# Performance work log

Measured on AMD Instinct MI355X. Metric: run time of the kernel, lower is better.

The kernel has to match this reference:

```python
import jax, jax.numpy as jnp
import numpy as np

N = 50176
E = 802816
G = 64
IN_DIM = 128
HID = 128
GLOB = 16
BN_EPS = 1e-5


def transformer_conv(x, src, dst, Wq, bq, Wk, bk, Wv, bv, Ws, bs):
    # PyG TransformerConv, heads=1, concat=True, root_weight=True, beta=False
    q = x @ Wq + bq          # [N, H]
    k = x @ Wk + bk          # [N, H]
    v = x @ Wv + bv          # [N, H]
    scale = 1.0 / jnp.sqrt(jnp.asarray(HID, x.dtype))
    logits = jnp.sum(q[dst] * k[src], axis=-1) * scale          # [E]
    m = jax.ops.segment_max(logits, dst, num_segments=N)        # [N]
    m = jnp.where(jnp.isfinite(m), m, 0.0)
    e = jnp.exp(logits - m[dst])                                # [E]
    s = jax.ops.segment_sum(e, dst, num_segments=N)             # [N]
    alpha = e / (s[dst] + 1e-16)                                # [E]
    agg = jax.ops.segment_sum(alpha[:, None] * v[src], dst, num_segments=N)
    return agg + x @ Ws + bs


def batch_norm(x, gamma, beta):
    mu = jnp.mean(x, axis=0)
    var = jnp.mean((x - mu) ** 2, axis=0)
    return gamma * (x - mu) / jnp.sqrt(var + BN_EPS) + beta


def setup_inputs() -> dict:
    key = jax.random.key(0)
    ks = jax.random.split(key, 32)
    d = {}
    d['x'] = jax.random.normal(ks[0], (N, IN_DIM), dtype=jnp.float32)
    d['edge_index'] = jax.random.randint(ks[1], (2, E), 0, N, dtype=jnp.int32)
    d['ptr'] = (jnp.arange(G + 1, dtype=jnp.int32) * (N // G))
    d['global_features'] = jax.random.normal(ks[2], (G, GLOB), dtype=jnp.float32)
    dims = [(IN_DIM, HID), (HID, HID)]
    ki = 3
    for l, (di, do) in enumerate(dims):
        for nm in ['Wq', 'Wk', 'Wv', 'Ws']:
            d[f'{nm}{l}'] = jax.random.normal(ks[ki], (di, do), dtype=jnp.float32) * 0.05; ki += 1
        for nm in ['bq', 'bk', 'bv', 'bs']:
            d[f'{nm}{l}'] = jnp.zeros((do,), dtype=jnp.float32)
        d[f'g{l}'] = jnp.ones((do,), dtype=jnp.float32)
        d[f'be{l}'] = jnp.zeros((do,), dtype=jnp.float32)
    d['fcW'] = jax.random.normal(ks[ki], (HID + GLOB, HID), dtype=jnp.float32) * 0.05; ki += 1
    d['fcb'] = jnp.zeros((HID,), dtype=jnp.float32)
    d['fc2W'] = jax.random.normal(ks[ki], (HID, 1), dtype=jnp.float32) * 0.05; ki += 1
    d['fc2b'] = jnp.zeros((1,), dtype=jnp.float32)
    return d


def reference(x, edge_index, ptr, global_features,
              Wq0, Wk0, Wv0, Ws0, bq0, bk0, bv0, bs0, g0, be0,
              Wq1, Wk1, Wv1, Ws1, bq1, bk1, bv1, bs1, g1, be1,
              fcW, fcb, fc2W, fc2b):
    src, dst = edge_index[0], edge_index[1]
    h = transformer_conv(x, src, dst, Wq0, bq0, Wk0, bk0, Wv0, bv0, Ws0, bs0)
    h = jax.nn.relu(batch_norm(h, g0, be0))
    h = transformer_conv(h, src, dst, Wq1, bq1, Wk1, bk1, Wv1, bv1, Ws1, bs1)
    h = jax.nn.relu(batch_norm(h, g1, be1))
    # broadcast per-graph global features to nodes using ptr boundaries
    graph_id = jnp.searchsorted(ptr, jnp.arange(N, dtype=ptr.dtype), side='right') - 1
    rep = global_features[graph_id]                              # [N, GLOB]
    h = jnp.concatenate([h, rep], axis=1)
    h = jax.nn.relu(h @ fcW + fcb)
    out = h @ fc2W + fc2b                                        # [N, 1]
    return out[:, 0]
```

## Files before the change

kernel.cpp:

```cpp
#include <hip/hip_runtime.h>
#include <math.h>

#define N_NODES 50176
#define N_EDGES 802816
#define HIDDEN  128
#define NGRAPH  64
#define BN_EPS  1e-5f
#define ATT_SCALE 0.08838834764831845f

typedef __attribute__((ext_vector_type(8))) short bf16x8;
typedef __attribute__((ext_vector_type(4))) float f32x4;

__device__ __forceinline__ float bflo(unsigned u) { return __uint_as_float(u << 16); }
__device__ __forceinline__ float bfhi(unsigned u) { return __uint_as_float(u & 0xffff0000u); }
__device__ __forceinline__ unsigned short f2bf(float f) {
    unsigned u = __float_as_uint(f);
    unsigned r = (u + 0x7fffu + ((u >> 16) & 1u)) >> 16;
    return (unsigned short)r;
}

__global__ void hist_kernel(const int* __restrict__ dst, int* __restrict__ cnt) {
    int e = blockIdx.x * 256 + threadIdx.x;
    if (e < N_EDGES) atomicAdd(&cnt[dst[e]], 1);
}

__global__ void scan1_kernel(const int* __restrict__ cnt, int* __restrict__ row_ptr,
                             int* __restrict__ bsum) {
    __shared__ int sh[256];
    int t = threadIdx.x, b = blockIdx.x;
    int base = b * 1024 + t * 4;
    int v0 = cnt[base], v1 = cnt[base + 1], v2 = cnt[base + 2], v3 = cnt[base + 3];
    int tot = v0 + v1 + v2 + v3;
    sh[t] = tot; __syncthreads();
    for (int off = 1; off < 256; off <<= 1) {
        int x = (t >= off) ? sh[t - off] : 0;
        __syncthreads();
        sh[t] += x;
        __syncthreads();
    }
    int excl = sh[t] - tot;
    row_ptr[base]     = excl;
    row_ptr[base + 1] = excl + v0;
    row_ptr[base + 2] = excl + v0 + v1;
    row_ptr[base + 3] = excl + v0 + v1 + v2;
    if (t == 255) bsum[b] = sh[255];
}

__global__ void scan2_kernel(const int* __restrict__ bsum, int* __restrict__ boff,
                             int* __restrict__ row_ptr) {
    int acc = 0;
    for (int i = 0; i < 49; i++) { boff[i] = acc; acc += bsum[i]; }
    row_ptr[N_NODES] = acc;
}

__global__ void scan3_kernel(int* __restrict__ row_ptr, int* __restrict__ cur,
                             const int* __restrict__ boff) {
    int t = threadIdx.x, b = blockIdx.x;
    int base = b * 1024 + t * 4;
    int off = boff[b];
    #pragma unroll
    for (int j = 0; j < 4; j++) {
        int v = row_ptr[base + j] + off;
        row_ptr[base + j] = v;
        cur[base + j] = v;
    }
}

__global__ void scatter_kernel(const int* __restrict__ src, const int* __restrict__ dst,
                               int* __restrict__ cur, int* __restrict__ edge_src) {
    int e = blockIdx.x * 256 + threadIdx.x;
    if (e < N_EDGES) {
        int d = dst[e];
        int slot = atomicAdd(&cur[d], 1);
        edge_src[slot] = src[e];
    }
}

__global__ void wprep_kernel(const float* __restrict__ Wq, const float* __restrict__ Wk,
                             const float* __restrict__ Wv, const float* __restrict__ Ws,
                             unsigned short* __restrict__ WT) {
    int mb = blockIdx.x;
    const float* W = (mb == 0) ? Wq : (mb == 1) ? Wk : (mb == 2) ? Wv : Ws;
    int t = threadIdx.x;
    int k = t >> 1, ch = t & 1;
    #pragma unroll 8
    for (int cc = 0; cc < 64; cc++) {
        int c = ch * 64 + cc;
        WT[((size_t)mb * 128 + c) * 128 + k] = f2bf(W[k * 128 + c]);
    }
}

__global__ __launch_bounds__(512, 4) void gemm_mfma(
    const float* __restrict__ in,
    const unsigned short* __restrict__ WT,
    const float* __restrict__ bq, const float* __restrict__ bk,
    const float* __restrict__ bv, const float* __restrict__ bs,
    float* __restrict__ qb, unsigned short* __restrict__ kvb,
    float* __restrict__ hb,
    const float* __restrict__ bnA, const float* __restrict__ bnB)
{
    __shared__ unsigned char ldsA[16384];
    __shared__ unsigned char ldsKV[32768];
    int t = threadIdx.x;
    int n0 = blockIdx.x * 64;

    {
        int r = t >> 3, seg = t & 7;
        const float* srcp = in + (size_t)(n0 + r) * 128 + seg * 16;
        float4 f0 = *reinterpret_cast<const float4*>(srcp);
        float4 f1 = *reinterpret_cast<const float4*>(srcp + 4);
        float4 f2 = *reinterpret_cast<const float4*>(srcp + 8);
        float4 f3 = *reinterpret_cast<const float4*>(srcp + 12);
        if (bnA) {
            int kb = seg * 16;
            float4 a0 = *reinterpret_cast<const float4*>(&bnA[kb]);
            float4 a1 = *reinterpret_cast<const float4*>(&bnA[kb + 4]);
            float4 a2 = *reinterpret_cast<const float4*>(&bnA[kb + 8]);
            float4 a3 = *reinterpret_cast<const float4*>(&bnA[kb + 12]);
            float4 b0 = *reinterpret_cast<const float4*>(&bnB[kb]);
            float4 b1 = *reinterpret_cast<const float4*>(&bnB[kb + 4]);
            float4 b2 = *reinterpret_cast<const float4*>(&bnB[kb + 8]);
            float4 b3 = *reinterpret_cast<const float4*>(&bnB[kb + 12]);
            f0.x = fmaxf(f0.x * a0.x + b0.x, 0.f); f0.y = fmaxf(f0.y * a0.y + b0.y, 0.f);
            f0.z = fmaxf(f0.z * a0.z + b0.z, 0.f); f0.w = fmaxf(f0.w * a0.w + b0.w, 0.f);
            f1.x = fmaxf(f1.x * a1.x + b1.x, 0.f); f1.y = fmaxf(f1.y * a1.y + b1.y, 0.f);
            f1.z = fmaxf(f1.z * a1.z + b1.z, 0.f); f1.w = fmaxf(f1.w * a1.w + b1.w, 0.f);
            f2.x = fmaxf(f2.x * a2.x + b2.x, 0.f); f2.y = fmaxf(f2.y * a2.y + b2.y, 0.f);
            f2.z = fmaxf(f2.z * a2.z + b2.z, 0.f); f2.w = fmaxf(f2.w * a2.w + b2.w, 0.f);
            f3.x = fmaxf(f3.x * a3.x + b3.x, 0.f); f3.y = fmaxf(f3.y * a3.y + b3.y, 0.f);
            f3.z = fmaxf(f3.z * a3.z + b3.z, 0.f); f3.w = fmaxf(f3.w * a3.w + b3.w, 0.f);
        }
        uint4 p0, p1;
        p0.x = (unsigned)f2bf(f0.x) | ((unsigned)f2bf(f0.y) << 16);
        p0.y = (unsigned)f2bf(f0.z) | ((unsigned)f2bf(f0.w) << 16);
        p0.z = (unsigned)f2bf(f1.x) | ((unsigned)f2bf(f1.y) << 16);
        p0.w = (unsigned)f2bf(f1.z) | ((unsigned)f2bf(f1.w) << 16);
        p1.x = (unsigned)f2bf(f2.x) | ((unsigned)f2bf(f2.y) << 16);
        p1.y = (unsigned)f2bf(f2.z) | ((unsigned)f2bf(f2.w) << 16);
        p1.z = (unsigned)f2bf(f3.x) | ((unsigned)f2bf(f3.y) << 16);
        p1.w = (unsigned)f2bf(f3.z) | ((unsigned)f2bf(f3.w) << 16);
        unsigned sw = (unsigned)((r & 7) << 4);
        *reinterpret_cast<uint4*>(&ldsA[r * 256 + (((unsigned)(seg * 32)) ^ sw)]) = p0;
        *reinterpret_cast<uint4*>(&ldsA[r * 256 + (((unsigned)(seg * 32 + 16)) ^ sw)]) = p1;
    }
    __syncthreads();

    int lane = t & 63, w = t >> 6;
    int m = w >> 1, half = w & 1;
    int lrow = lane & 15, lk = lane >> 4;

    f32x4 acc[4][4] = {};
    #pragma unroll
    for (int ks = 0; ks < 4; ks++) {
        bf16x8 bfr[4], af[4];
        #pragma unroll
        for (int j = 0; j < 4; j++) {
            int col = half * 64 + j * 16 + lrow;
            bfr[j] = *reinterpret_cast<const bf16x8*>(
                &WT[((size_t)m * 128 + col) * 128 + ks * 32 + lk * 8]);
        }
        #pragma unroll
        for (int i = 0; i < 4; i++) {
            unsigned row = (unsigned)(i * 16 + lrow);
            af[i] = *reinterpret_cast<const bf16x8*>(
                &ldsA[row * 256 + (((unsigned)(ks * 64 + lk * 16)) ^ ((row & 7) << 4))]);
        }
        #pragma unroll
        for (int i = 0; i < 4; i++)
            #pragma unroll
            for (int j = 0; j < 4; j++)
                acc[i][j] = __builtin_amdgcn_mfma_f32_16x16x32_bf16(af[i], bfr[j], acc[i][j], 0, 0, 0);
    }

    const float* bias = (m == 0) ? bq : (m == 1) ? bk : (m == 2) ? bv : bs;
    if (m == 0 || m == 3) {
        float* ob = (m == 0) ? qb : hb;
        #pragma unroll
        for (int j = 0; j < 4; j++) {
            int c = half * 64 + j * 16 + lrow;
            float bi = bias[c];
            #pragma unroll
            for (int i = 0; i < 4; i++)
                #pragma unroll
                for (int r4 = 0; r4 < 4; r4++) {
                    int row = n0 + i * 16 + lk * 4 + r4;
                    ob[(size_t)row * 128 + c] = acc[i][j][r4] + bi;
                }
        }
    } else {
        unsigned vOff = (m == 1) ? 0u : 256u;
        #pragma unroll
        for (int j = 0; j < 4; j++) {
            int c = half * 64 + j * 16 + lrow;
            float bi = bias[c];
            unsigned bir = vOff + (unsigned)c * 2;
            #pragma unroll
            for (int i = 0; i < 4; i++)
                #pragma unroll
                for (int r4 = 0; r4 < 4; r4++) {
                    unsigned row = (unsigned)(i * 16 + lk * 4 + r4);
                    unsigned sw = ((row >> 2) & 3) << 5;
                    *reinterpret_cast<unsigned short*>(&ldsKV[row * 512 + (bir ^ sw)]) =
                        f2bf(acc[i][j][r4] + bi);
                }
        }
    }
    __syncthreads();
    {
        int r = t >> 3, seg = t & 7;
        unsigned sw = (((unsigned)r >> 2) & 3) << 5;
        char* dst = (char*)(kvb + (size_t)(n0 + r) * 256) + seg * 64;
        #pragma unroll
        for (int u = 0; u < 4; u++) {
            uint4 v = *reinterpret_cast<const uint4*>(
                &ldsKV[r * 512 + (((unsigned)(seg * 64 + u * 16)) ^ sw)]);
            *reinterpret_cast<uint4*>(dst + u * 16) = v;
        }
    }
}

__global__ __launch_bounds__(256) void agg_kernel(
    const float* __restrict__ qb, const unsigned short* __restrict__ kvb,
    const int* __restrict__ row_ptr, const int* __restrict__ edge_src,
    float* __restrict__ hb)
{
    int wave = threadIdx.x >> 6, lane = threadIdx.x & 63;
    int n = blockIdx.x * 4 + wave;
    int quarter = lane >> 4, ql = lane & 15;

    float4 qa = *reinterpret_cast<const float4*>(&qb[(size_t)n * 128 + ql * 8]);
    float4 qc = *reinterpret_cast<const float4*>(&qb[(size_t)n * 128 + ql * 8 + 4]);
    int s0 = row_ptr[n], s1 = row_ptr[n + 1];

    float acc0 = 0.f, acc1 = 0.f, acc2 = 0.f, acc3 = 0.f;
    float acc4 = 0.f, acc5 = 0.f, acc6 = 0.f, acc7 = 0.f;
    float ssum = 0.f;

    for (int j0 = s0; j0 < s1; j0 += 4) {
        int j = j0 + quarter;
        bool act = (j < s1);
        int s = act ? edge_src[j] : 0;
        const uint4* kv4 = reinterpret_cast<const uint4*>(kvb + (size_t)s * 256);
        uint4 kr = kv4[ql];
        uint4 vr = kv4[16 + ql];

        float part = qa.x * bflo(kr.x) + qa.y * bfhi(kr.x)
                   + qa.z * bflo(kr.y) + qa.w * bfhi(kr.y)
                   + qc.x * bflo(kr.z) + qc.y * bfhi(kr.z)
                   + qc.z * bflo(kr.w) + qc.w * bfhi(kr.w);
        part += __shfl_xor(part, 1, 64);
        part += __shfl_xor(part, 2, 64);
        part += __shfl_xor(part, 4, 64);
        part += __shfl_xor(part, 8, 64);

        float wgt = act ? __expf(part * ATT_SCALE) : 0.f;
        ssum += wgt;
        acc0 += wgt * bflo(vr.x); acc1 += wgt * bfhi(vr.x);
        acc2 += wgt * bflo(vr.y); acc3 += wgt * bfhi(vr.y);
        acc4 += wgt * bflo(vr.z); acc5 += wgt * bfhi(vr.z);
        acc6 += wgt * bflo(vr.w); acc7 += wgt * bfhi(vr.w);
    }

    #define XRED(x) { x += __shfl_xor(x, 16, 64); x += __shfl_xor(x, 32, 64); }
    XRED(acc0) XRED(acc1) XRED(acc2) XRED(acc3)
    XRED(acc4) XRED(acc5) XRED(acc6) XRED(acc7)
    XRED(ssum)
    #undef XRED

    if (quarter == 0) {
        float inv = 1.0f / (ssum + 1e-16f);
        float4 h0 = *reinterpret_cast<float4*>(&hb[(size_t)n * 128 + ql * 8]);
        float4 h1 = *reinterpret_cast<float4*>(&hb[(size_t)n * 128 + ql * 8 + 4]);
        h0.x += acc0 * inv; h0.y += acc1 * inv; h0.z += acc2 * inv; h0.w += acc3 * inv;
        h1.x += acc4 * inv; h1.y += acc5 * inv; h1.z += acc6 * inv; h1.w += acc7 * inv;
        *reinterpret_cast<float4*>(&hb[(size_t)n * 128 + ql * 8]) = h0;
        *reinterpret_cast<float4*>(&hb[(size_t)n * 128 + ql * 8 + 4]) = h1;
    }
}

__global__ __launch_bounds__(256) void bn_stats(const float* __restrict__ h,
                                                float* __restrict__ sums,
                                                float* __restrict__ sqs) {
    int t = threadIdx.x;
    int c = t & 127;
    float s = 0.f, q = 0.f;
    int stride = gridDim.x * 256;
    for (int i = blockIdx.x * 256 + t; i < N_NODES * 128; i += stride) {
        float v = h[i];
        s += v; q += v * v;
    }
    __shared__ float sh[256], shq[256];
    sh[t] = s; shq[t] = q;
    __syncthreads();
    if (t < 128) {
        atomicAdd(&sums[c], sh[t] + sh[t + 128]);
        atomicAdd(&sqs[c],  shq[t] + shq[t + 128]);
    }
}

__global__ void bn_final(const float* __restrict__ sums, const float* __restrict__ sqs,
                         const float* __restrict__ g, const float* __restrict__ be,
                         float* __restrict__ a, float* __restrict__ b) {
    int c = threadIdx.x;
    float mean = sums[c] / (float)N_NODES;
    float var  = sqs[c] / (float)N_NODES - mean * mean;
    float inv  = rsqrtf(var + BN_EPS);
    float av   = g[c] * inv;
    a[c] = av;
    b[c] = be[c] - mean * av;
}

__global__ __launch_bounds__(256) void fc_kernel(
    const float* __restrict__ h2, const float* __restrict__ a1, const float* __restrict__ b1,
    const int* __restrict__ ptr, const float* __restrict__ gf,
    const float* __restrict__ fcW, const float* __restrict__ fcb,
    const float* __restrict__ fc2W, const float* __restrict__ fc2b,
    float* __restrict__ out)
{
    __shared__ float hc[8][144];
    __shared__ float red[8][128];
    int t = threadIdx.x;
    int nb = blockIdx.x * 8;

    {
        int node_l = t >> 5, li = t & 31;
        int n = nb + node_l;
        float4 v = *reinterpret_cast<const float4*>(&h2[(size_t)n * 128 + li * 4]);
        float4 av = *reinterpret_cast<const float4*>(&a1[li * 4]);
        float4 bv = *reinterpret_cast<const float4*>(&b1[li * 4]);
        hc[node_l][li * 4 + 0] = fmaxf(v.x * av.x + bv.x, 0.f);
        hc[node_l][li * 4 + 1] = fmaxf(v.y * av.y + bv.y, 0.f);
        hc[node_l][li * 4 + 2] = fmaxf(v.z * av.z + bv.z, 0.f);
        hc[node_l][li * 4 + 3] = fmaxf(v.w * av.w + bv.w, 0.f);
        if (li < 16) {
            int lo = 0, hi = NGRAPH;
            while (lo < hi) {
                int mid = (lo + hi + 1) >> 1;
                if (ptr[mid] <= n) lo = mid; else hi = mid - 1;
            }
            hc[node_l][128 + li] = gf[lo * 16 + li];
        }
    }
    __syncthreads();

    {
        int half = t >> 7, o = t & 127;
        float fb = fcb[o];
        float acc0 = fb, acc1 = fb, acc2 = fb, acc3 = fb;
        const float* h0 = hc[half * 4 + 0];
        const float* h1 = hc[half * 4 + 1];
        const float* h2c = hc[half * 4 + 2];
        const float* h3 = hc[half * 4 + 3];
        #pragma unroll 16
        for (int i = 0; i < 144; i++) {
            float w = fcW[i * 128 + o];
            acc0 += h0[i] * w;
            acc1 += h1[i] * w;
            acc2 += h2c[i] * w;
            acc3 += h3[i] * w;
        }
        float w2 = fc2W[o];
        red[half * 4 + 0][o] = fmaxf(acc0, 0.f) * w2;
        red[half * 4 + 1][o] = fmaxf(acc1, 0.f) * w2;
        red[half * 4 + 2][o] = fmaxf(acc2, 0.f) * w2;
        red[half * 4 + 3][o] = fmaxf(acc3, 0.f) * w2;
    }
    __syncthreads();

    {
        int node_l = t >> 5, li = t & 31;
        float s = red[node_l][li] + red[node_l][li + 32]
                + red[node_l][li + 64] + red[node_l][li + 96];
        s += __shfl_xor(s, 1, 64);
        s += __shfl_xor(s, 2, 64);
        s += __shfl_xor(s, 4, 64);
        s += __shfl_xor(s, 8, 64);
        s += __shfl_xor(s, 16, 64);
        if (li == 0) out[nb + node_l] = s + fc2b[0];
    }
}

extern "C" void kernel_launch(void* const* d_in, const int* in_sizes, int n_in,
                              void* d_out, int out_size, void* d_ws, size_t ws_size,
                              hipStream_t stream)
{
    const float* x   = (const float*)d_in[0];
    const int*   ei  = (const int*)d_in[1];
    const int*   ptr = (const int*)d_in[2];
    const float* gf  = (const float*)d_in[3];
    const float* Wq0 = (const float*)d_in[4];
    const float* Wk0 = (const float*)d_in[5];
    const float* Wv0 = (const float*)d_in[6];
    const float* Ws0 = (const float*)d_in[7];
    const float* bq0 = (const float*)d_in[8];
    const float* bk0 = (const float*)d_in[9];
    const float* bv0 = (const float*)d_in[10];
    const float* bs0 = (const float*)d_in[11];
    const float* g0  = (const float*)d_in[12];
    const float* be0 = (const float*)d_in[13];
    const float* Wq1 = (const float*)d_in[14];
    const float* Wk1 = (const float*)d_in[15];
    const float* Wv1 = (const float*)d_in[16];
    const float* Ws1 = (const float*)d_in[17];
    const float* bq1 = (const float*)d_in[18];
    const float* bk1 = (const float*)d_in[19];
    const float* bv1 = (const float*)d_in[20];
    const float* bs1 = (const float*)d_in[21];
    const float* g1  = (const float*)d_in[22];
    const float* be1 = (const float*)d_in[23];
    const float* fcW = (const float*)d_in[24];
    const float* fcb = (const float*)d_in[25];
    const float* fc2W= (const float*)d_in[26];
    const float* fc2b= (const float*)d_in[27];
    float* out = (float*)d_out;

    const int* src_p = ei;
    const int* dst_p = ei + N_EDGES;

    char* w = (char*)d_ws;
    const size_t NM = (size_t)N_NODES * 128 * sizeof(float);
    float* qb = (float*)w;                    w += NM;
    unsigned short* kvb = (unsigned short*)w; w += (size_t)N_NODES * 256 * sizeof(unsigned short);
    float* h1 = (float*)w;                    w += NM;
    float* h2 = (float*)w;                    w += NM;
    float* stats = (float*)w;                 w += 1024 * sizeof(float);
    float* sums0 = stats;
    float* sqs0  = stats + 128;
    float* sums1 = stats + 256;
    float* sqs1  = stats + 384;
    float* a0    = stats + 512;
    float* b0    = stats + 640;
    float* a1    = stats + 768;
    float* b1    = stats + 896;
    unsigned short* WT0 = (unsigned short*)w; w += (size_t)512 * 128 * sizeof(unsigned short);
    unsigned short* WT1 = (unsigned short*)w; w += (size_t)512 * 128 * sizeof(unsigned short);
    int* cnt     = (int*)w;                   w += (size_t)N_NODES * sizeof(int);
    int* row_ptr = (int*)w;                   w += (size_t)(N_NODES + 1) * sizeof(int);
    int* cur     = (int*)w;                   w += (size_t)N_NODES * sizeof(int);
    int* edge_src= (int*)w;                   w += (size_t)N_EDGES * sizeof(int);
    int* bsum    = (int*)w;                   w += 64 * sizeof(int);
    int* boff    = (int*)w;                   w += 64 * sizeof(int);

    hipMemsetAsync(cnt, 0, (size_t)N_NODES * sizeof(int), stream);
    hipMemsetAsync(stats, 0, 512 * sizeof(float), stream);

    wprep_kernel<<<4, 256, 0, stream>>>(Wq0, Wk0, Wv0, Ws0, WT0);
    wprep_kernel<<<4, 256, 0, stream>>>(Wq1, Wk1, Wv1, Ws1, WT1);

    hist_kernel<<<3136, 256, 0, stream>>>(dst_p, cnt);
    scan1_kernel<<<49, 256, 0, stream>>>(cnt, row_ptr, bsum);
    scan2_kernel<<<1, 1, 0, stream>>>(bsum, boff, row_ptr);
    scan3_kernel<<<49, 256, 0, stream>>>(row_ptr, cur, boff);
    scatter_kernel<<<3136, 256, 0, stream>>>(src_p, dst_p, cur, edge_src);

    gemm_mfma<<<784, 512, 0, stream>>>(x, WT0,
        bq0, bk0, bv0, bs0, qb, kvb, h1, nullptr, nullptr);
    agg_kernel<<<12544, 256, 0, stream>>>(qb, kvb, row_ptr, edge_src, h1);
    bn_stats<<<784, 256, 0, stream>>>(h1, sums0, sqs0);
    bn_final<<<1, 128, 0, stream>>>(sums0, sqs0, g0, be0, a0, b0);

    gemm_mfma<<<784, 512, 0, stream>>>(h1, WT1,
        bq1, bk1, bv1, bs1, qb, kvb, h2, a0, b0);
    agg_kernel<<<12544, 256, 0, stream>>>(qb, kvb, row_ptr, edge_src, h2);
    bn_stats<<<784, 256, 0, stream>>>(h2, sums1, sqs1);
    bn_final<<<1, 128, 0, stream>>>(sums1, sqs1, g1, be1, a1, b1);

    fc_kernel<<<6272, 256, 0, stream>>>(h2, a1, b1, ptr, gf,
        fcW, fcb, fc2W, fc2b, out);
}
```

Before: 519.4 us.

## Store Q as bf16, unroll edge loop, fold BN-final and scan2 into consumers

Q is now written in bf16 through an LDS staging buffer with coalesced stores, which halves Q traffic in the aggregation kernel. The aggregation loop handles two edges per quarter-wave per iteration to expose more memory-level parallelism. The bn_final and scan2 kernels are removed: the BN affine coefficients are recomputed from the raw sums in the GEMM and FC kernels, and the block-offset scan is done with wave shuffles inside scan3. bn_stats now reads float4s. Lower Q precision slightly changes numerics, and the extra syncthreads in the GEMM epilogue adds a barrier.

```diff
diff --git a/kernel.cpp b/kernel.cpp
--- a/kernel.cpp
+++ b/kernel.cpp
@@ -17,6 +17,20 @@
     unsigned u = __float_as_uint(f);
     unsigned r = (u + 0x7fffu + ((u >> 16) & 1u)) >> 16;
     return (unsigned short)r;
+}
+
+__device__ __forceinline__ void bn_ab4(const float* __restrict__ S, const float* __restrict__ Q,
+                                       const float* __restrict__ G, const float* __restrict__ BE,
+                                       int c, float4& A, float4& B) {
+    const float invN = 1.0f / (float)N_NODES;
+    float4 s = *reinterpret_cast<const float4*>(&S[c]);
+    float4 q = *reinterpret_cast<const float4*>(&Q[c]);
+    float4 g = *reinterpret_cast<const float4*>(&G[c]);
+    float4 e = *reinterpret_cast<const float4*>(&BE[c]);
+    #define BNC(x) { float mu = s.x * invN; float va = q.x * invN - mu * mu; \
+                     float iv = rsqrtf(va + BN_EPS); A.x = g.x * iv; B.x = e.x - mu * A.x; }
+    BNC(x) BNC(y) BNC(z) BNC(w)
+    #undef BNC
 }
 
 __global__ void hist_kernel(const int* __restrict__ dst, int* __restrict__ cnt) {
@@ -46,18 +60,24 @@
     if (t == 255) bsum[b] = sh[255];
 }
 
-__global__ void scan2_kernel(const int* __restrict__ bsum, int* __restrict__ boff,
-                             int* __restrict__ row_ptr) {
-    int acc = 0;
-    for (int i = 0; i < 49; i++) { boff[i] = acc; acc += bsum[i]; }
-    row_ptr[N_NODES] = acc;
-}
-
 __global__ void scan3_kernel(int* __restrict__ row_ptr, int* __restrict__ cur,
-                             const int* __restrict__ boff) {
+                             const int* __restrict__ bsum) {
+    __shared__ int sh_off;
     int t = threadIdx.x, b = blockIdx.x;
+    if (t < 64) {
+        int v = (t < 49) ? bsum[t] : 0;
+        int inc = v;
+        #pragma unroll
+        for (int o = 1; o < 64; o <<= 1) {
+            int u = __shfl_up(inc, o, 64);
+            if (t >= o) inc += u;
+        }
+        if (t == b) sh_off = inc - v;
+        if (b == 48 && t == 48) row_ptr[N_NODES] = inc;
+    }
+    __syncthreads();
+    int off = sh_off;
     int base = b * 1024 + t * 4;
-    int off = boff[b];
     #pragma unroll
     for (int j = 0; j < 4; j++) {
         int v = row_ptr[base + j] + off;
@@ -95,9 +115,10 @@
     const unsigned short* __restrict__ WT,
     const float* __restrict__ bq, const float* __restrict__ bk,
     const float* __restrict__ bv, const float* __restrict__ bs,
-    float* __restrict__ qb, unsigned short* __restrict__ kvb,
+    unsigned short* __restrict__ qbf, unsigned short* __restrict__ kvb,
     float* __restrict__ hb,
-    const float* __restrict__ bnA, const float* __restrict__ bnB)
+    const float* __restrict__ bnS, const float* __restrict__ bnQ,
+    const float* __restrict__ bnG, const float* __restrict__ bnBe)
 {
     __shared__ unsigned char ldsA[16384];
     __shared__ unsigned char ldsKV[32768];
@@ -111,16 +132,13 @@
         float4 f1 = *reinterpret_cast<const float4*>(srcp + 4);
         float4 f2 = *reinterpret_cast<const float4*>(srcp + 8);
         float4 f3 = *reinterpret_cast<const float4*>(srcp + 12);
-        if (bnA) {
+        if (bnS) {
             int kb = seg * 16;
-            float4 a0 = *reinterpret_cast<const float4*>(&bnA[kb]);
-            float4 a1 = *reinterpret_cast<const float4*>(&bnA[kb + 4]);
-            float4 a2 = *reinterpret_cast<const float4*>(&bnA[kb + 8]);
-            float4 a3 = *reinterpret_cast<const float4*>(&bnA[kb + 12]);
-            float4 b0 = *reinterpret_cast<const float4*>(&bnB[kb]);
-            float4 b1 = *reinterpret_cast<const float4*>(&bnB[kb + 4]);
-            float4 b2 = *reinterpret_cast<const float4*>(&bnB[kb + 8]);
-            float4 b3 = *reinterpret_cast<const float4*>(&bnB[kb + 12]);
+            float4 a0, b0, a1, b1, a2, b2, a3, b3;
+            bn_ab4(bnS, bnQ, bnG, bnBe, kb,      a0, b0);
+            bn_ab4(bnS, bnQ, bnG, bnBe, kb + 4,  a1, b1);
+            bn_ab4(bnS, bnQ, bnG, bnBe, kb + 8,  a2, b2);
+            bn_ab4(bnS, bnQ, bnG, bnBe, kb + 12, a3, b3);
             f0.x = fmaxf(f0.x * a0.x + b0.x, 0.f); f0.y = fmaxf(f0.y * a0.y + b0.y, 0.f);
             f0.z = fmaxf(f0.z * a0.z + b0.z, 0.f); f0.w = fmaxf(f0.w * a0.w + b0.w, 0.f);
             f1.x = fmaxf(f1.x * a1.x + b1.x, 0.f); f1.y = fmaxf(f1.y * a1.y + b1.y, 0.f);
@@ -172,9 +190,10 @@
                 acc[i][j] = __builtin_amdgcn_mfma_f32_16x16x32_bf16(af[i], bfr[j], acc[i][j], 0, 0, 0);
     }
 
+    __syncthreads();
+
     const float* bias = (m == 0) ? bq : (m == 1) ? bk : (m == 2) ? bv : bs;
-    if (m == 0 || m == 3) {
-        float* ob = (m == 0) ? qb : hb;
+    if (m == 3) {
         #pragma unroll
         for (int j = 0; j < 4; j++) {
             int c = half * 64 + j * 16 + lrow;
@@ -184,7 +203,23 @@
                 #pragma unroll
                 for (int r4 = 0; r4 < 4; r4++) {
                     int row = n0 + i * 16 + lk * 4 + r4;
-                    ob[(size_t)row * 128 + c] = acc[i][j][r4] + bi;
+                    hb[(size_t)row * 128 + c] = acc[i][j][r4] + bi;
+                }
+        }
+    } else if (m == 0) {
+        #pragma unroll
+        for (int j = 0; j < 4; j++) {
+            int c = half * 64 + j * 16 + lrow;
+            float bi = bias[c];
+            #pragma unroll
+            for (int i = 0; i < 4; i++)
+                #pragma unroll
+                for (int r4 = 0; r4 < 4; r4++) {
+                    unsigned row = (unsigned)(i * 16 + lk * 4 + r4);
+                    unsigned sw = ((row >> 2) & 3) << 5;
+                    *reinterpret_cast<unsigned short*>(
+                        &ldsA[row * 256 + (((unsigned)(2 * c)) ^ sw)]) =
+                        f2bf(acc[i][j][r4] + bi);
                 }
         }
     } else {
@@ -206,9 +241,17 @@
         }
     }
     __syncthreads();
+
     {
         int r = t >> 3, seg = t & 7;
         unsigned sw = (((unsigned)r >> 2) & 3) << 5;
+        char* qdst = (char*)(qbf + (size_t)(n0 + r) * 128) + seg * 32;
+        uint4 v0 = *reinterpret_cast<const uint4*>(
+            &ldsA[r * 256 + (((unsigned)(seg * 32)) ^ sw)]);
+        uint4 v1 = *reinterpret_cast<const uint4*>(
+            &ldsA[r * 256 + ((((unsigned)(seg * 32)) ^ sw) + 16)]);
+        *reinterpret_cast<uint4*>(qdst) = v0;
+        *reinterpret_cast<uint4*>(qdst + 16) = v1;
         char* dst = (char*)(kvb + (size_t)(n0 + r) * 256) + seg * 64;
         #pragma unroll
         for (int u = 0; u < 4; u++) {
@@ -220,7 +263,7 @@
 }
 
 __global__ __launch_bounds__(256) void agg_kernel(
-    const float* __restrict__ qb, const unsigned short* __restrict__ kvb,
+    const unsigned short* __restrict__ qbf, const unsigned short* __restrict__ kvb,
     const int* __restrict__ row_ptr, const int* __restrict__ edge_src,
     float* __restrict__ hb)
 {
@@ -228,38 +271,48 @@
     int n = blockIdx.x * 4 + wave;
     int quarter = lane >> 4, ql = lane & 15;
 
-    float4 qa = *reinterpret_cast<const float4*>(&qb[(size_t)n * 128 + ql * 8]);
-    float4 qc = *reinterpret_cast<const float4*>(&qb[(size_t)n * 128 + ql * 8 + 4]);
+    uint4 qr = reinterpret_cast<const uint4*>(qbf + (size_t)n * 128)[ql];
+    float q0 = bflo(qr.x), q1 = bfhi(qr.x), q2 = bflo(qr.y), q3 = bfhi(qr.y);
+    float q4v = bflo(qr.z), q5 = bfhi(qr.z), q6 = bflo(qr.w), q7 = bfhi(qr.w);
+
     int s0 = row_ptr[n], s1 = row_ptr[n + 1];
 
     float acc0 = 0.f, acc1 = 0.f, acc2 = 0.f, acc3 = 0.f;
     float acc4 = 0.f, acc5 = 0.f, acc6 = 0.f, acc7 = 0.f;
     float ssum = 0.f;
 
-    for (int j0 = s0; j0 < s1; j0 += 4) {
-        int j = j0 + quarter;
-        bool act = (j < s1);
-        int s = act ? edge_src[j] : 0;
-        const uint4* kv4 = reinterpret_cast<const uint4*>(kvb + (size_t)s * 256);
-        uint4 kr = kv4[ql];
-        uint4 vr = kv4[16 + ql];
-
-        float part = qa.x * bflo(kr.x) + qa.y * bfhi(kr.x)
-                   + qa.z * bflo(kr.y) + qa.w * bfhi(kr.y)
-                   + qc.x * bflo(kr.z) + qc.y * bfhi(kr.z)
-                   + qc.z * bflo(kr.w) + qc.w * bfhi(kr.w);
-        part += __shfl_xor(part, 1, 64);
-        part += __shfl_xor(part, 2, 64);
-        part += __shfl_xor(part, 4, 64);
-        part += __shfl_xor(part, 8, 64);
-
-        float wgt = act ? __expf(part * ATT_SCALE) : 0.f;
-        ssum += wgt;
-        acc0 += wgt * bflo(vr.x); acc1 += wgt * bfhi(vr.x);
-        acc2 += wgt * bflo(vr.y); acc3 += wgt * bfhi(vr.y);
-        acc4 += wgt * bflo(vr.z); acc5 += wgt * bfhi(vr.z);
-        acc6 += wgt * bflo(vr.w); acc7 += wgt * bfhi(vr.w);
-    }
+    #define EDGE_ACC(kr, vr, act)                                          \
+    {                                                                      \
+        float part = q0 * bflo(kr.x) + q1 * bfhi(kr.x)                     \
+                   + q2 * bflo(kr.y) + q3 * bfhi(kr.y)                     \
+                   + q4v * bflo(kr.z) + q5 * bfhi(kr.z)                    \
+                   + q6 * bflo(kr.w) + q7 * bfhi(kr.w);                    \
+        part += __shfl_xor(part, 1, 64);                                   \
+        part += __shfl_xor(part, 2, 64);                                   \
+        part += __shfl_xor(part, 4, 64);                                   \
+        part += __shfl_xor(part, 8, 64);                                   \
+        float wgt = (act) ? __expf(part * ATT_SCALE) : 0.f;                \
+        ssum += wgt;                                                       \
+        acc0 += wgt * bflo(vr.x); acc1 += wgt * bfhi(vr.x);                \
+        acc2 += wgt * bflo(vr.y); acc3 += wgt * bfhi(vr.y);                \
+        acc4 += wgt * bflo(vr.z); acc5 += wgt * bfhi(vr.z);                \
+        acc6 += wgt * bflo(vr.w); acc7 += wgt * bfhi(vr.w);                \
+    }
+
+    for (int j0 = s0; j0 < s1; j0 += 8) {
+        int ja = j0 + quarter;
+        int jb = ja + 4;
+        bool aa = ja < s1, ab = jb < s1;
+        int sa = aa ? edge_src[ja] : 0;
+        int sb = ab ? edge_src[jb] : 0;
+        const uint4* pa = reinterpret_cast<const uint4*>(kvb + (size_t)sa * 256);
+        const uint4* pb = reinterpret_cast<const uint4*>(kvb + (size_t)sb * 256);
+        uint4 kra = pa[ql], vra = pa[16 + ql];
+        uint4 krb = pb[ql], vrb = pb[16 + ql];
+        EDGE_ACC(kra, vra, aa)
+        EDGE_ACC(krb, vrb, ab)
+    }
+    #undef EDGE_ACC
 
     #define XRED(x) { x += __shfl_xor(x, 16, 64); x += __shfl_xor(x, 32, 64); }
     XRED(acc0) XRED(acc1) XRED(acc2) XRED(acc3)
@@ -282,36 +335,31 @@
                                                 float* __restrict__ sums,
                                                 float* __restrict__ sqs) {
     int t = threadIdx.x;
-    int c = t & 127;
-    float s = 0.f, q = 0.f;
-    int stride = gridDim.x * 256;
-    for (int i = blockIdx.x * 256 + t; i < N_NODES * 128; i += stride) {
-        float v = h[i];
-        s += v; q += v * v;
-    }
-    __shared__ float sh[256], shq[256];
-    sh[t] = s; shq[t] = q;
+    float4 s4 = make_float4(0.f, 0.f, 0.f, 0.f);
+    float4 q4 = make_float4(0.f, 0.f, 0.f, 0.f);
+    const int stride = 784 * 256;
+    for (int i = blockIdx.x * 256 + t; i < N_NODES * 32; i += stride) {
+        float4 v = reinterpret_cast<const float4*>(h)[i];
+        s4.x += v.x; s4.y += v.y; s4.z += v.z; s4.w += v.w;
+        q4.x += v.x * v.x; q4.y += v.y * v.y; q4.z += v.z * v.z; q4.w += v.w * v.w;
+    }
+    __shared__ float sh_s[1024], sh_q[1024];
+    sh_s[t * 4 + 0] = s4.x; sh_s[t * 4 + 1] = s4.y; sh_s[t * 4 + 2] = s4.z; sh_s[t * 4 + 3] = s4.w;
+    sh_q[t * 4 + 0] = q4.x; sh_q[t * 4 + 1] = q4.y; sh_q[t * 4 + 2] = q4.z; sh_q[t * 4 + 3] = q4.w;
     __syncthreads();
     if (t < 128) {
-        atomicAdd(&sums[c], sh[t] + sh[t + 128]);
-        atomicAdd(&sqs[c],  shq[t] + shq[t + 128]);
-    }
-}
-
-__global__ void bn_final(const float* __restrict__ sums, const float* __restrict__ sqs,
-                         const float* __restrict__ g, const float* __restrict__ be,
-                         float* __restrict__ a, float* __restrict__ b) {
-    int c = threadIdx.x;
-    float mean = sums[c] / (float)N_NODES;
-    float var  = sqs[c] / (float)N_NODES - mean * mean;
-    float inv  = rsqrtf(var + BN_EPS);
-    float av   = g[c] * inv;
-    a[c] = av;
-    b[c] = be[c] - mean * av;
+        float ss = 0.f, qq = 0.f;
+        #pragma unroll
+        for (int r = 0; r < 8; r++) { ss += sh_s[t + 128 * r]; qq += sh_q[t + 128 * r]; }
+        atomicAdd(&sums[t], ss);
+        atomicAdd(&sqs[t], qq);
+    }
 }
 
 __global__ __launch_bounds__(256) void fc_kernel(
-    const float* __restrict__ h2, const float* __restrict__ a1, const float* __restrict__ b1,
+    const float* __restrict__ h2,
+    const float* __restrict__ bnS, const float* __restrict__ bnQ,
+    const float* __restrict__ bnG, const float* __restrict__ bnBe,
     const int* __restrict__ ptr, const float* __restrict__ gf,
     const float* __restrict__ fcW, const float* __restrict__ fcb,
     const float* __restrict__ fc2W, const float* __restrict__ fc2b,
@@ -326,8 +374,8 @@
         int node_l = t >> 5, li = t & 31;
         int n = nb + node_l;
         float4 v = *reinterpret_cast<const float4*>(&h2[(size_t)n * 128 + li * 4]);
-        float4 av = *reinterpret_cast<const float4*>(&a1[li * 4]);
-        float4 bv = *reinterpret_cast<const float4*>(&b1[li * 4]);
+        float4 av, bv;
+        bn_ab4(bnS, bnQ, bnG, bnBe, li * 4, av, bv);
         hc[node_l][li * 4 + 0] = fmaxf(v.x * av.x + bv.x, 0.f);
         hc[node_l][li * 4 + 1] = fmaxf(v.y * av.y + bv.y, 0.f);
         hc[node_l][li * 4 + 2] = fmaxf(v.z * av.z + bv.z, 0.f);
@@ -419,27 +467,22 @@
 
     char* w = (char*)d_ws;
     const size_t NM = (size_t)N_NODES * 128 * sizeof(float);
-    float* qb = (float*)w;                    w += NM;
-    unsigned short* kvb = (unsigned short*)w; w += (size_t)N_NODES * 256 * sizeof(unsigned short);
-    float* h1 = (float*)w;                    w += NM;
-    float* h2 = (float*)w;                    w += NM;
-    float* stats = (float*)w;                 w += 1024 * sizeof(float);
+    unsigned short* qbf = (unsigned short*)w;  w += (size_t)N_NODES * 128 * sizeof(unsigned short);
+    unsigned short* kvb = (unsigned short*)w;  w += (size_t)N_NODES * 256 * sizeof(unsigned short);
+    float* h1 = (float*)w;                     w += NM;
+    float* h2 = (float*)w;                     w += NM;
+    float* stats = (float*)w;                  w += 512 * sizeof(float);
     float* sums0 = stats;
     float* sqs0  = stats + 128;
     float* sums1 = stats + 256;
     float* sqs1  = stats + 384;
-    float* a0    = stats + 512;
-    float* b0    = stats + 640;
-    float* a1    = stats + 768;
-    float* b1    = stats + 896;
-    unsigned short* WT0 = (unsigned short*)w; w += (size_t)512 * 128 * sizeof(unsigned short);
-    unsigned short* WT1 = (unsigned short*)w; w += (size_t)512 * 128 * sizeof(unsigned short);
-    int* cnt     = (int*)w;                   w += (size_t)N_NODES * sizeof(int);
-    int* row_ptr = (int*)w;                   w += (size_t)(N_NODES + 1) * sizeof(int);
-    int* cur     = (int*)w;                   w += (size_t)N_NODES * sizeof(int);
-    int* edge_src= (int*)w;                   w += (size_t)N_EDGES * sizeof(int);
-    int* bsum    = (int*)w;                   w += 64 * sizeof(int);
-    int* boff    = (int*)w;                   w += 64 * sizeof(int);
+    unsigned short* WT0 = (unsigned short*)w;  w += (size_t)512 * 128 * sizeof(unsigned short);
+    unsigned short* WT1 = (unsigned short*)w;  w += (size_t)512 * 128 * sizeof(unsigned short);
+    int* cnt     = (int*)w;                    w += (size_t)N_NODES * sizeof(int);
+    int* row_ptr = (int*)w;                    w += (size_t)(N_NODES + 1) * sizeof(int);
+    int* cur     = (int*)w;                    w += (size_t)N_NODES * sizeof(int);
+    int* edge_src= (int*)w;                    w += (size_t)N_EDGES * sizeof(int);
+    int* bsum    = (int*)w;                    w += 64 * sizeof(int);
 
     hipMemsetAsync(cnt, 0, (size_t)N_NODES * sizeof(int), stream);
     hipMemsetAsync(stats, 0, 512 * sizeof(float), stream);
@@ -449,22 +492,19 @@
 
     hist_kernel<<<3136, 256, 0, stream>>>(dst_p, cnt);
     scan1_kernel<<<49, 256, 0, stream>>>(cnt, row_ptr, bsum);
-    scan2_kernel<<<1, 1, 0, stream>>>(bsum, boff, row_ptr);
-    scan3_kernel<<<49, 256, 0, stream>>>(row_ptr, cur, boff);
+    scan3_kernel<<<49, 256, 0, stream>>>(row_ptr, cur, bsum);
     scatter_kernel<<<3136, 256, 0, stream>>>(src_p, dst_p, cur, edge_src);
 
     gemm_mfma<<<784, 512, 0, stream>>>(x, WT0,
-        bq0, bk0, bv0, bs0, qb, kvb, h1, nullptr, nullptr);
-    agg_kernel<<<12544, 256, 0, stream>>>(qb, kvb, row_ptr, edge_src, h1);
+        bq0, bk0, bv0, bs0, qbf, kvb, h1, nullptr, nullptr, nullptr, nullptr);
+    agg_kernel<<<12544, 256, 0, stream>>>(qbf, kvb, row_ptr, edge_src, h1);
     bn_stats<<<784, 256, 0, stream>>>(h1, sums0, sqs0);
-    bn_final<<<1, 128, 0, stream>>>(sums0, sqs0, g0, be0, a0, b0);
 
     gemm_mfma<<<784, 512, 0, stream>>>(h1, WT1,
-        bq1, bk1, bv1, bs1, qb, kvb, h2, a0, b0);
-    agg_kernel<<<12544, 256, 0, stream>>>(qb, kvb, row_ptr, edge_src, h2);
+        bq1, bk1, bv1, bs1, qbf, kvb, h2, sums0, sqs0, g0, be0);
+    agg_kernel<<<12544, 256, 0, stream>>>(qbf, kvb, row_ptr, edge_src, h2);
     bn_stats<<<784, 256, 0, stream>>>(h2, sums1, sqs1);
-    bn_final<<<1, 128, 0, stream>>>(sums1, sqs1, g1, be1, a1, b1);
-
-    fc_kernel<<<6272, 256, 0, stream>>>(h2, a1, b1, ptr, gf,
+
+    fc_kernel<<<6272, 256, 0, stream>>>(h2, sums1, sqs1, g1, be1, ptr, gf,
         fcW, fcb, fc2W, fc2b, out);
 }
```

Result: no change. 509.5 us (-1.9%).
